# Performance work log

Hardware: AMD Instinct MI355X
Metric: run time of the kernel (lower is better)

The kernel has to match this reference:

```python
import jax, jax.numpy as jnp
import numpy as np

DIM = 128
HEADS = 4
DIM_HEAD = 32
HIDDEN = HEADS * DIM_HEAD  # 128
EPS = 1e-5


def setup_inputs() -> dict:
    key = jax.random.key(0)
    k0, k1, k2, k3 = jax.random.split(key, 4)
    b, h, w = 8, 128, 128
    x = jax.random.normal(k0, (b, DIM, h, w), dtype=jnp.float32)
    # 1x1 conv weights stored as [out_ch, in_ch]
    w_qkv = jax.random.normal(k1, (HIDDEN * 3, DIM), dtype=jnp.float32) * (1.0 / np.sqrt(DIM))
    w_out = jax.random.normal(k2, (DIM, HIDDEN), dtype=jnp.float32) * (1.0 / np.sqrt(HIDDEN))
    b_out = jnp.zeros((DIM,), dtype=jnp.float32)
    alpha = jnp.ones((DIM,), dtype=jnp.float32)
    beta = jnp.zeros((DIM,), dtype=jnp.float32)
    return {"x": x, "w_qkv": w_qkv, "w_out": w_out, "b_out": b_out,
            "alpha": alpha, "beta": beta}


def reference(x, w_qkv, w_out, b_out, alpha, beta):
    b, c, h, w = x.shape
    n = h * w
    scale = DIM_HEAD ** (-0.5)
    # 1x1 conv QKV (bias=False) == channel GEMM
    qkv = jnp.einsum('bchw,oc->bohw', x, w_qkv)  # [b, 3*HIDDEN, h, w]
    q, k, v = jnp.split(qkv, 3, axis=1)
    rs = lambda t: t.reshape(b, HEADS, DIM_HEAD, n)  # [b, heads, d, N]
    q = jax.nn.softmax(rs(q), axis=-2) * scale  # softmax over dim_head axis
    k = jax.nn.softmax(rs(k), axis=-1)          # softmax over spatial axis
    v = rs(v) / n
    # context[dk, dv] = sum_n k[dk, n] * v[dv, n]   (tiny d x d matrix)
    context = jnp.einsum('bhkn,bhvn->bhkv', k, v)
    # out[dv, n] = sum_dk context[dk, dv] * q[dk, n]
    out = jnp.einsum('bhkv,bhkn->bhvn', context, q)
    out = out.reshape(b, HIDDEN, h, w)
    # to_out: 1x1 conv with bias, then channel LayerNorm
    out = jnp.einsum('bchw,oc->bohw', out, w_out) + b_out[None, :, None, None]
    mean = jnp.mean(out, axis=1, keepdims=True)
    var = jnp.var(out, axis=1, keepdims=True)  # unbiased=False
    out = (out - mean) / jnp.sqrt(var + EPS)
    return out * alpha[None, :, None, None] + beta[None, :, None, None]
```

## Files before the change

kernel.cpp:

```cpp
#include <hip/hip_runtime.h>
#include <math.h>

#define B_ 8
#define C_ 128
#define N_ 16384
#define SCALE_ 0.17677669529663687f
#define EPS_ 1e-5f

#define KV_STRIDE 36
#define XU_STRIDE 68
#define REC_ 4224

typedef _Float16 half8 __attribute__((ext_vector_type(8)));
typedef float floatx4 __attribute__((ext_vector_type(4)));

static __device__ inline unsigned short f16bits(float v) {
  _Float16 h = (_Float16)v;
  return __builtin_bit_cast(unsigned short, h);
}

static __device__ inline void pack2(float a0, float a1,
                                    unsigned int& hp, unsigned int& lp) {
  _Float16 h0 = (_Float16)a0;
  _Float16 h1 = (_Float16)a1;
  float l0f = (a0 - (float)h0) * 2048.0f;
  float l1f = (a1 - (float)h1) * 2048.0f;
  hp = ((unsigned int)__builtin_bit_cast(unsigned short, h1) << 16) |
       (unsigned int)__builtin_bit_cast(unsigned short, h0);
  lp = ((unsigned int)f16bits(l1f) << 16) | (unsigned int)f16bits(l0f);
}

static __device__ inline void split8(const float* p, half8& hi, half8& lo) {
  float4 f0 = *(const float4*)p;
  float4 f1 = *(const float4*)(p + 4);
  float fv[8] = {f0.x, f0.y, f0.z, f0.w, f1.x, f1.y, f1.z, f1.w};
#pragma unroll
  for (int j = 0; j < 8; ++j) {
    _Float16 hj = (_Float16)fv[j];
    hi[j] = hj;
    lo[j] = (_Float16)((fv[j] - (float)hj) * 2048.0f);
  }
}

__global__ __launch_bounds__(1024, 4) void lin_attn_ctx(
    const float* __restrict__ x, const float* __restrict__ wqkv,
    float* __restrict__ Ws)
{
  __shared__ __align__(16) unsigned int xhiu[32 * XU_STRIDE];
  __shared__ __align__(16) unsigned int xlou[32 * XU_STRIDE];
  __shared__ __align__(16) float ks[128 * KV_STRIDE];
  __shared__ __align__(16) float vs[128 * KV_STRIDE];

  const int t = threadIdx.x;
  const int bpb = gridDim.x / B_;
  const int b = blockIdx.x / bpb;
  const int blk = blockIdx.x - b * bpb;
  const int nchunks = 512 / bpb;
  const int pbase = blk * (nchunks << 5);

  const int lane = t & 63;
  const int wave = t >> 6;
  const int l15 = lane & 15;
  const int quad = lane >> 4;

  half8 ahi[4], alo[4];
#pragma unroll
  for (int s = 0; s < 4; ++s)
    split8(wqkv + (size_t)(128 + (wave << 4) + l15) * C_ + (s << 5) + (quad << 3),
           ahi[s], alo[s]);

  const int hj = wave >> 2;
  const int at = (wave >> 1) & 1;
  const int bt = wave & 1;
  floatx4 pacc1 = (floatx4){0.f, 0.f, 0.f, 0.f};
  floatx4 pacc2 = (floatx4){0.f, 0.f, 0.f, 0.f};
  float sacc[4] = {0.f, 0.f, 0.f, 0.f};

  const float* xb = x + ((size_t)b * C_) * N_;
  const int kp0 = t >> 4;
  const int pq0 = (t & 15) << 1;

  float2 fa0, fa1;
  {
    const float* p = xb + pbase + pq0;
    fa0 = *(const float2*)(p + (size_t)(2 * kp0) * N_);
    fa1 = *(const float2*)(p + (size_t)(2 * kp0 + 1) * N_);
  }

  for (int c4 = 0; c4 < nchunks; ++c4) {
    __syncthreads();

    half8 eh, el, vh, vl;
    if (c4 > 0) {
      split8(&ks[((hj << 5) + (at << 4) + l15) * KV_STRIDE + (quad << 3)], eh, el);
      split8(&vs[((hj << 5) + (bt << 4) + l15) * KV_STRIDE + (quad << 3)], vh, vl);
    }

    {
      float a0[2] = {fa0.x, fa0.y};
      float a1[2] = {fa1.x, fa1.y};
#pragma unroll
      for (int j = 0; j < 2; ++j) {
        unsigned int hp, lp;
        pack2(a0[j], a1[j], hp, lp);
        xhiu[(pq0 + j) * XU_STRIDE + kp0] = hp;
        xlou[(pq0 + j) * XU_STRIDE + kp0] = lp;
      }
    }

    if (c4 > 0) {
      pacc1 = __builtin_amdgcn_mfma_f32_16x16x32_f16(eh, vh, pacc1, 0, 0, 0);
      pacc2 = __builtin_amdgcn_mfma_f32_16x16x32_f16(eh, vl, pacc2, 0, 0, 0);
      pacc2 = __builtin_amdgcn_mfma_f32_16x16x32_f16(el, vh, pacc2, 0, 0, 0);
    }

    __syncthreads();

    if (c4 + 1 < nchunks) {
      const float* p = xb + pbase + ((c4 + 1) << 5) + pq0;
      fa0 = *(const float2*)(p + (size_t)(2 * kp0) * N_);
      fa1 = *(const float2*)(p + (size_t)(2 * kp0 + 1) * N_);
    }

    floatx4 acc1[2], acc2[2];
#pragma unroll
    for (int c = 0; c < 2; ++c) {
      acc1[c] = (floatx4){0.f, 0.f, 0.f, 0.f};
      acc2[c] = (floatx4){0.f, 0.f, 0.f, 0.f};
    }
    __builtin_amdgcn_s_setprio(1);
#pragma unroll
    for (int s = 0; s < 4; ++s) {
#pragma unroll
      for (int c = 0; c < 2; ++c) {
        int off = ((c << 4) + l15) * XU_STRIDE + (s << 4) + (quad << 2);
        half8 bh = __builtin_bit_cast(half8, *(const uint4*)&xhiu[off]);
        half8 bl = __builtin_bit_cast(half8, *(const uint4*)&xlou[off]);
        acc1[c] = __builtin_amdgcn_mfma_f32_16x16x32_f16(ahi[s], bh, acc1[c], 0, 0, 0);
        acc2[c] = __builtin_amdgcn_mfma_f32_16x16x32_f16(ahi[s], bl, acc2[c], 0, 0, 0);
        acc2[c] = __builtin_amdgcn_mfma_f32_16x16x32_f16(alo[s], bh, acc2[c], 0, 0, 0);
      }
    }
    __builtin_amdgcn_s_setprio(0);

    if (wave < 8) {
#pragma unroll
      for (int c = 0; c < 2; ++c) {
        int px = (c << 4) + l15;
#pragma unroll
        for (int reg = 0; reg < 4; ++reg) {
          float val = acc1[c][reg] + acc2[c][reg] * (1.0f / 2048.0f);
          int row = (wave << 4) + (quad << 2) + reg;
          float e = __expf(val);
          ks[row * KV_STRIDE + px] = e;
          sacc[reg] += e;
        }
      }
    } else {
#pragma unroll
      for (int c = 0; c < 2; ++c) {
        int px = (c << 4) + l15;
#pragma unroll
        for (int reg = 0; reg < 4; ++reg) {
          float val = acc1[c][reg] + acc2[c][reg] * (1.0f / 2048.0f);
          int row = ((wave - 8) << 4) + (quad << 2) + reg;
          vs[row * KV_STRIDE + px] = val;
        }
      }
    }
  }

  __syncthreads();
  {
    half8 eh, el, vh, vl;
    split8(&ks[((hj << 5) + (at << 4) + l15) * KV_STRIDE + (quad << 3)], eh, el);
    split8(&vs[((hj << 5) + (bt << 4) + l15) * KV_STRIDE + (quad << 3)], vh, vl);
    pacc1 = __builtin_amdgcn_mfma_f32_16x16x32_f16(eh, vh, pacc1, 0, 0, 0);
    pacc2 = __builtin_amdgcn_mfma_f32_16x16x32_f16(eh, vl, pacc2, 0, 0, 0);
    pacc2 = __builtin_amdgcn_mfma_f32_16x16x32_f16(el, vh, pacc2, 0, 0, 0);
  }

  {
    float* rec = Ws + (size_t)blockIdx.x * REC_;
#pragma unroll
    for (int reg = 0; reg < 4; ++reg) {
      int dk = (at << 4) + (quad << 2) + reg;
      int dv = (bt << 4) + l15;
      rec[(((hj << 5) + dk) << 5) + dv] =
          pacc1[reg] + pacc2[reg] * (1.0f / 2048.0f);
    }
    if (wave < 8) {
#pragma unroll
      for (int reg = 0; reg < 4; ++reg) {
        float s = sacc[reg];
        s += __shfl_xor(s, 1);
        s += __shfl_xor(s, 2);
        s += __shfl_xor(s, 4);
        s += __shfl_xor(s, 8);
        sacc[reg] = s;
      }
      if (l15 == 0) {
#pragma unroll
        for (int reg = 0; reg < 4; ++reg)
          rec[4096 + (wave << 4) + (quad << 2) + reg] = sacc[reg];
      }
    }
  }
}

__global__ void lin_attn_redg(const float* __restrict__ Ws, int slots,
                              const float* __restrict__ wout,
                              float* __restrict__ G)
{
  __shared__ float p2[256];
  __shared__ float cx[128];
  __shared__ float ss[4];

  const int t = threadIdx.x;
  const int b = blockIdx.x >> 5;
  const int seg = blockIdx.x & 31;
  const int R0 = seg << 2;
  const int hs = slots >> 1;

  {
    const int e = t & 127;
    const int half = t >> 7;
    const float* src = Ws + ((size_t)b * slots + (size_t)half * hs) * REC_ +
                       R0 * 32 + e;
    float s = 0.f;
    for (int k = 0; k < hs; ++k) s += src[(size_t)k * REC_];
    p2[half * 128 + e] = s;
  }
  {
    const int row4 = t >> 6;
    const int lane = t & 63;
    float sv = (lane < slots)
             ? Ws[((size_t)b * slots + lane) * REC_ + 4096 + R0 + row4] : 0.f;
    sv += __shfl_xor(sv, 1);
    sv += __shfl_xor(sv, 2);
    sv += __shfl_xor(sv, 4);
    sv += __shfl_xor(sv, 8);
    sv += __shfl_xor(sv, 16);
    sv += __shfl_xor(sv, 32);
    if (lane == 0) ss[row4] = sv;
  }
  __syncthreads();
  if (t < 128) {
    cx[t] = (p2[t] + p2[128 + t]) / (ss[t >> 5] * 16384.f);
  }
  __syncthreads();
  {
    const int o = t >> 1;
    const int pr = t & 1;
#pragma unroll
    for (int p = 0; p < 2; ++p) {
      const int row4 = pr * 2 + p;
      const int grow = R0 + row4;
      const int h = grow >> 5;
      const float* wrow = wout + (size_t)o * 128 + h * 32;
      const float* crow = &cx[row4 * 32];
      float s = 0.f;
#pragma unroll
      for (int q = 0; q < 8; ++q) {
        float4 w4 = *(const float4*)&wrow[q * 4];
        float4 c4 = *(const float4*)&crow[q * 4];
        s += w4.x * c4.x + w4.y * c4.y + w4.z * c4.z + w4.w * c4.w;
      }
      G[(size_t)b * 16384 + (size_t)o * 128 + grow] = s * SCALE_;
    }
  }
}

__global__ __launch_bounds__(1024, 4) void lin_attn_out(
    const float* __restrict__ x, const float* __restrict__ wqkv,
    const float* __restrict__ G, const float* __restrict__ bout,
    const float* __restrict__ alpha, const float* __restrict__ beta,
    float* __restrict__ out)
{
  __shared__ __align__(16) unsigned int xh[2][32 * XU_STRIDE];
  __shared__ __align__(16) unsigned int xl[2][32 * XU_STRIDE];
  __shared__ __align__(16) unsigned int qhiu[32 * XU_STRIDE];
  __shared__ __align__(16) unsigned int qlou[32 * XU_STRIDE];
  __shared__ float ssum[256];
  __shared__ float red_s[2][256];
  __shared__ float red_q[2][256];

  const int t = threadIdx.x;
  const int bpb = gridDim.x / B_;
  const int b = blockIdx.x / bpb;
  const int blk = blockIdx.x - b * bpb;
  const int nchunks = 512 / bpb;
  const int pbase = blk * (nchunks << 5);

  const int lane = t & 63;
  const int wave = t >> 6;
  const int l15 = lane & 15;
  const int quad = lane >> 4;
  const bool qw = (wave < 8);
  const int yw = wave - 8;

  half8 ahi[4], alo[4];
  {
    const float* base = qw
        ? (wqkv + (size_t)((wave << 4) + l15) * C_)
        : (G + (size_t)b * 16384 + (size_t)((yw << 4) + l15) * 128);
#pragma unroll
    for (int s = 0; s < 4; ++s)
      split8(base + (s << 5) + (quad << 3), ahi[s], alo[s]);
  }

  float bch[4], ach[4], bech[4];
  if (!qw) {
#pragma unroll
    for (int reg = 0; reg < 4; ++reg) {
      int ch = (yw << 4) + (quad << 2) + reg;
      bch[reg] = bout[ch];
      ach[reg] = alpha[ch];
      bech[reg] = beta[ch];
    }
  }

  const float* xb = x + ((size_t)b * C_) * N_;
  float* ob0 = out + ((size_t)b * C_) * N_ + pbase;
  const int kp0 = t >> 4;
  const int pq0 = (t & 15) << 1;

  float2 fa0, fa1;
  {
    const float* p = xb + pbase + pq0;
    fa0 = *(const float2*)(p + (size_t)(2 * kp0) * N_);
    fa1 = *(const float2*)(p + (size_t)(2 * kp0 + 1) * N_);
    float a0[2] = {fa0.x, fa0.y};
    float a1[2] = {fa1.x, fa1.y};
#pragma unroll
    for (int j = 0; j < 2; ++j) {
      unsigned int hp, lp;
      pack2(a0[j], a1[j], hp, lp);
      xh[0][(pq0 + j) * XU_STRIDE + kp0] = hp;
      xl[0][(pq0 + j) * XU_STRIDE + kp0] = lp;
    }
  }

  float eq[2][4];
  float sown[2];
  float yv[2][4];

  for (int i = 0; i <= nchunks; ++i) {
    __syncthreads();

    if (i + 1 < nchunks) {
      const float* p = xb + pbase + ((i + 1) << 5) + pq0;
      fa0 = *(const float2*)(p + (size_t)(2 * kp0) * N_);
      fa1 = *(const float2*)(p + (size_t)(2 * kp0 + 1) * N_);
    }

    if (qw) {
      if (i < nchunks) {
        const int cur = i & 1;
        floatx4 a1c[2], a2c[2];
#pragma unroll
        for (int c = 0; c < 2; ++c) {
          a1c[c] = (floatx4){0.f, 0.f, 0.f, 0.f};
          a2c[c] = (floatx4){0.f, 0.f, 0.f, 0.f};
        }
        __builtin_amdgcn_s_setprio(1);
#pragma unroll
        for (int s = 0; s < 4; ++s) {
#pragma unroll
          for (int c = 0; c < 2; ++c) {
            int off = ((c << 4) + l15) * XU_STRIDE + (s << 4) + (quad << 2);
            half8 bh = __builtin_bit_cast(half8, *(const uint4*)&xh[cur][off]);
            half8 bl = __builtin_bit_cast(half8, *(const uint4*)&xl[cur][off]);
            a1c[c] = __builtin_amdgcn_mfma_f32_16x16x32_f16(ahi[s], bh, a1c[c], 0, 0, 0);
            a2c[c] = __builtin_amdgcn_mfma_f32_16x16x32_f16(ahi[s], bl, a2c[c], 0, 0, 0);
            a2c[c] = __builtin_amdgcn_mfma_f32_16x16x32_f16(alo[s], bh, a2c[c], 0, 0, 0);
          }
        }
        __builtin_amdgcn_s_setprio(0);
#pragma unroll
        for (int c = 0; c < 2; ++c) {
          float s4 = 0.f;
#pragma unroll
          for (int reg = 0; reg < 4; ++reg) {
            float v = a1c[c][reg] + a2c[c][reg] * (1.0f / 2048.0f);
            float e = __expf(v);
            eq[c][reg] = e;
            s4 += e;
          }
          s4 += __shfl_xor(s4, 16);
          s4 += __shfl_xor(s4, 32);
          sown[c] = s4;
          if (quad == 0) ssum[(wave << 5) + (c << 4) + l15] = s4;
        }
      }
    } else {
      if (i >= 2) {
        const float* rs = red_s[i & 1];
        const float* rq = red_q[i & 1];
        float* ob = ob0 + ((i - 2) << 5);
#pragma unroll
        for (int c = 0; c < 2; ++c) {
          int px = (c << 4) + l15;
          float ts = ((rs[px] + rs[32 + px]) + (rs[64 + px] + rs[96 + px])) +
                     ((rs[128 + px] + rs[160 + px]) + (rs[192 + px] + rs[224 + px]));
          float tq = ((rq[px] + rq[32 + px]) + (rq[64 + px] + rq[96 + px])) +
                     ((rq[128 + px] + rq[160 + px]) + (rq[192 + px] + rq[224 + px]));
          float mean = ts * (1.f / 128.f);
          float var = tq * (1.f / 128.f) - mean * mean;
          float rstd = 1.f / sqrtf(var + EPS_);
#pragma unroll
          for (int reg = 0; reg < 4; ++reg) {
            int ch = (yw << 4) + (quad << 2) + reg;
            ob[(size_t)ch * N_ + px] =
                (yv[c][reg] - mean) * rstd * ach[reg] + bech[reg];
          }
        }
      }
      if (i >= 1) {
        floatx4 a1c[2], a2c[2];
#pragma unroll
        for (int c = 0; c < 2; ++c) {
          a1c[c] = (floatx4){0.f, 0.f, 0.f, 0.f};
          a2c[c] = (floatx4){0.f, 0.f, 0.f, 0.f};
        }
        __builtin_amdgcn_s_setprio(1);
#pragma unroll
        for (int s = 0; s < 4; ++s) {
#pragma unroll
          for (int c = 0; c < 2; ++c) {
            int off = ((c << 4) + l15) * XU_STRIDE + (s << 4) + (quad << 2);
            half8 bh = __builtin_bit_cast(half8, *(const uint4*)&qhiu[off]);
            half8 bl = __builtin_bit_cast(half8, *(const uint4*)&qlou[off]);
            a1c[c] = __builtin_amdgcn_mfma_f32_16x16x32_f16(ahi[s], bh, a1c[c], 0, 0, 0);
            a2c[c] = __builtin_amdgcn_mfma_f32_16x16x32_f16(ahi[s], bl, a2c[c], 0, 0, 0);
            a2c[c] = __builtin_amdgcn_mfma_f32_16x16x32_f16(alo[s], bh, a2c[c], 0, 0, 0);
          }
        }
        __builtin_amdgcn_s_setprio(0);
        const int cb = (i - 1) & 1;
#pragma unroll
        for (int c = 0; c < 2; ++c) {
          float sm = 0.f, sq = 0.f;
#pragma unroll
          for (int reg = 0; reg < 4; ++reg) {
            float v = a1c[c][reg] + a2c[c][reg] * (1.0f / 2048.0f) + bch[reg];
            yv[c][reg] = v;
            sm += v;
            sq += v * v;
          }
          sm += __shfl_xor(sm, 16);  sq += __shfl_xor(sq, 16);
          sm += __shfl_xor(sm, 32);  sq += __shfl_xor(sq, 32);
          if (quad == 0) {
            red_s[cb][(yw << 5) + (c << 4) + l15] = sm;
            red_q[cb][(yw << 5) + (c << 4) + l15] = sq;
          }
        }
      }
    }

    if (i + 1 < nchunks) {
      const int nx = (i + 1) & 1;
      float a0[2] = {fa0.x, fa0.y};
      float a1[2] = {fa1.x, fa1.y};
#pragma unroll
      for (int j = 0; j < 2; ++j) {
        unsigned int hp, lp;
        pack2(a0[j], a1[j], hp, lp);
        xh[nx][(pq0 + j) * XU_STRIDE + kp0] = hp;
        xl[nx][(pq0 + j) * XU_STRIDE + kp0] = lp;
      }
    }

    __syncthreads();

    if (qw && i < nchunks) {
#pragma unroll
      for (int c = 0; c < 2; ++c) {
        int px = (c << 4) + l15;
        float pairs = ssum[((wave ^ 1) << 5) + (c << 4) + l15];
        float inv = 1.0f / (sown[c] + pairs);
        unsigned int h0, l0, h1, l1;
        pack2(eq[c][0] * inv, eq[c][1] * inv, h0, l0);
        pack2(eq[c][2] * inv, eq[c][3] * inv, h1, l1);
        int kp = (wave << 3) + (quad << 1);
        uint2 hu; hu.x = h0; hu.y = h1;
        uint2 lu; lu.x = l0; lu.y = l1;
        *(uint2*)&qhiu[px * XU_STRIDE + kp] = hu;
        *(uint2*)&qlou[px * XU_STRIDE + kp] = lu;
      }
    }
  }

  __syncthreads();
  if (!qw) {
    const float* rs = red_s[(nchunks - 1) & 1];
    const float* rq = red_q[(nchunks - 1) & 1];
    float* ob = ob0 + ((nchunks - 1) << 5);
#pragma unroll
    for (int c = 0; c < 2; ++c) {
      int px = (c << 4) + l15;
      float ts = ((rs[px] + rs[32 + px]) + (rs[64 + px] + rs[96 + px])) +
                 ((rs[128 + px] + rs[160 + px]) + (rs[192 + px] + rs[224 + px]));
      float tq = ((rq[px] + rq[32 + px]) + (rq[64 + px] + rq[96 + px])) +
                 ((rq[128 + px] + rq[160 + px]) + (rq[192 + px] + rq[224 + px]));
      float mean = ts * (1.f / 128.f);
      float var = tq * (1.f / 128.f) - mean * mean;
      float rstd = 1.f / sqrtf(var + EPS_);
#pragma unroll
      for (int reg = 0; reg < 4; ++reg) {
        int ch = (yw << 4) + (quad << 2) + reg;
        ob[(size_t)ch * N_ + px] =
            (yv[c][reg] - mean) * rstd * ach[reg] + bech[reg];
      }
    }
  }
}

extern "C" void kernel_launch(void* const* d_in, const int* in_sizes, int n_in,
                              void* d_out, int out_size, void* d_ws, size_t ws_size,
                              hipStream_t stream) {
  const float* x     = (const float*)d_in[0];
  const float* wqkv  = (const float*)d_in[1];
  const float* wout  = (const float*)d_in[2];
  const float* bout  = (const float*)d_in[3];
  const float* alpha = (const float*)d_in[4];
  const float* beta  = (const float*)d_in[5];
  float* outp = (float*)d_out;

  float* G  = (float*)d_ws;
  float* Ws = G + (size_t)B_ * 16384 + B_ * 4096 + B_ * 128;

  const int bpb_ctx = 32;

  lin_attn_ctx<<<dim3(B_ * bpb_ctx), dim3(1024), 0, stream>>>(x, wqkv, Ws);
  lin_attn_redg<<<dim3(B_ * 32), dim3(256), 0, stream>>>(Ws, bpb_ctx, wout, G);
  lin_attn_out<<<dim3(B_ * 32), dim3(1024), 0, stream>>>(x, wqkv, G, bout,
                                                         alpha, beta, outp);
}
```

Baseline: 212.2 us.

## Deepen chunk pipeline to one barrier per iteration with double-buffered q tiles

Restructures the main loop of the output kernel so each chunk iteration needs only one __syncthreads instead of two. The q-normalisation store moves to the start of the next iteration, and the q tiles and softmax partial sums become double-buffered. The pipeline grows by one stage, so the output-GEMM and LayerNorm waves lag two chunks behind. The x staging loads are also narrowed to the upper 512 threads, each doing float4 loads, which frees the q-softmax waves from global load work. In exchange the kernel uses more LDS and runs extra drain iterations, which may reduce occupancy.

```diff
diff --git a/kernel.cpp b/kernel.cpp
--- a/kernel.cpp
+++ b/kernel.cpp
@@ -279,9 +279,9 @@
 {
   __shared__ __align__(16) unsigned int xh[2][32 * XU_STRIDE];
   __shared__ __align__(16) unsigned int xl[2][32 * XU_STRIDE];
-  __shared__ __align__(16) unsigned int qhiu[32 * XU_STRIDE];
-  __shared__ __align__(16) unsigned int qlou[32 * XU_STRIDE];
-  __shared__ float ssum[256];
+  __shared__ __align__(16) unsigned int qh[2][32 * XU_STRIDE];
+  __shared__ __align__(16) unsigned int ql[2][32 * XU_STRIDE];
+  __shared__ float ssum[2][256];
   __shared__ float red_s[2][256];
   __shared__ float red_q[2][256];
 
@@ -322,18 +322,20 @@
 
   const float* xb = x + ((size_t)b * C_) * N_;
   float* ob0 = out + ((size_t)b * C_) * N_ + pbase;
-  const int kp0 = t >> 4;
-  const int pq0 = (t & 15) << 1;
-
-  float2 fa0, fa1;
-  {
+
+  const int st = t - 512;
+  const int kp0 = st >> 3;
+  const int pq0 = (st & 7) << 2;
+
+  float4 fa0, fa1;
+  if (t >= 512) {
     const float* p = xb + pbase + pq0;
-    fa0 = *(const float2*)(p + (size_t)(2 * kp0) * N_);
-    fa1 = *(const float2*)(p + (size_t)(2 * kp0 + 1) * N_);
-    float a0[2] = {fa0.x, fa0.y};
-    float a1[2] = {fa1.x, fa1.y};
-#pragma unroll
-    for (int j = 0; j < 2; ++j) {
+    fa0 = *(const float4*)(p + (size_t)(2 * kp0) * N_);
+    fa1 = *(const float4*)(p + (size_t)(2 * kp0 + 1) * N_);
+    float a0[4] = {fa0.x, fa0.y, fa0.z, fa0.w};
+    float a1[4] = {fa1.x, fa1.y, fa1.z, fa1.w};
+#pragma unroll
+    for (int j = 0; j < 4; ++j) {
       unsigned int hp, lp;
       pack2(a0[j], a1[j], hp, lp);
       xh[0][(pq0 + j) * XU_STRIDE + kp0] = hp;
@@ -345,16 +347,33 @@
   float sown[2];
   float yv[2][4];
 
-  for (int i = 0; i <= nchunks; ++i) {
+  for (int i = 0; i <= nchunks + 2; ++i) {
     __syncthreads();
 
-    if (i + 1 < nchunks) {
+    if (t >= 512 && i + 1 < nchunks) {
       const float* p = xb + pbase + ((i + 1) << 5) + pq0;
-      fa0 = *(const float2*)(p + (size_t)(2 * kp0) * N_);
-      fa1 = *(const float2*)(p + (size_t)(2 * kp0 + 1) * N_);
+      fa0 = *(const float4*)(p + (size_t)(2 * kp0) * N_);
+      fa1 = *(const float4*)(p + (size_t)(2 * kp0 + 1) * N_);
     }
 
     if (qw) {
+      if (i >= 1 && i - 1 < nchunks) {
+        const int pe = (i - 1) & 1;
+#pragma unroll
+        for (int c = 0; c < 2; ++c) {
+          int px = (c << 4) + l15;
+          float pairs = ssum[pe][((wave ^ 1) << 5) + (c << 4) + l15];
+          float inv = 1.0f / (sown[c] + pairs);
+          unsigned int h0, l0, h1, l1;
+          pack2(eq[c][0] * inv, eq[c][1] * inv, h0, l0);
+          pack2(eq[c][2] * inv, eq[c][3] * inv, h1, l1);
+          int kp = (wave << 3) + (quad << 1);
+          uint2 hu; hu.x = h0; hu.y = h1;
+          uint2 lu; lu.x = l0; lu.y = l1;
+          *(uint2*)&qh[pe][px * XU_STRIDE + kp] = hu;
+          *(uint2*)&ql[pe][px * XU_STRIDE + kp] = lu;
+        }
+      }
       if (i < nchunks) {
         const int cur = i & 1;
         floatx4 a1c[2], a2c[2];
@@ -390,14 +409,15 @@
           s4 += __shfl_xor(s4, 16);
           s4 += __shfl_xor(s4, 32);
           sown[c] = s4;
-          if (quad == 0) ssum[(wave << 5) + (c << 4) + l15] = s4;
+          if (quad == 0) ssum[i & 1][(wave << 5) + (c << 4) + l15] = s4;
         }
       }
     } else {
-      if (i >= 2) {
-        const float* rs = red_s[i & 1];
-        const float* rq = red_q[i & 1];
-        float* ob = ob0 + ((i - 2) << 5);
+      if (i >= 3) {
+        const int pf = (i - 3) & 1;
+        const float* rs = red_s[pf];
+        const float* rq = red_q[pf];
+        float* ob = ob0 + ((i - 3) << 5);
 #pragma unroll
         for (int c = 0; c < 2; ++c) {
           int px = (c << 4) + l15;
@@ -416,7 +436,8 @@
           }
         }
       }
-      if (i >= 1) {
+      if (i >= 2 && i - 2 < nchunks) {
+        const int pe = i & 1;
         floatx4 a1c[2], a2c[2];
 #pragma unroll
         for (int c = 0; c < 2; ++c) {
@@ -429,15 +450,14 @@
 #pragma unroll
           for (int c = 0; c < 2; ++c) {
             int off = ((c << 4) + l15) * XU_STRIDE + (s << 4) + (quad << 2);
-            half8 bh = __builtin_bit_cast(half8, *(const uint4*)&qhiu[off]);
-            half8 bl = __builtin_bit_cast(half8, *(const uint4*)&qlou[off]);
+            half8 bh = __builtin_bit_cast(half8, *(const uint4*)&qh[pe][off]);
+            half8 bl = __builtin_bit_cast(half8, *(const uint4*)&ql[pe][off]);
             a1c[c] = __builtin_amdgcn_mfma_f32_16x16x32_f16(ahi[s], bh, a1c[c], 0, 0, 0);
             a2c[c] = __builtin_amdgcn_mfma_f32_16x16x32_f16(ahi[s], bl, a2c[c], 0, 0, 0);
             a2c[c] = __builtin_amdgcn_mfma_f32_16x16x32_f16(alo[s], bh, a2c[c], 0, 0, 0);
           }
         }
         __builtin_amdgcn_s_setprio(0);
-        const int cb = (i - 1) & 1;
 #pragma unroll
         for (int c = 0; c < 2; ++c) {
           float sm = 0.f, sq = 0.f;
@@ -451,66 +471,23 @@
           sm += __shfl_xor(sm, 16);  sq += __shfl_xor(sq, 16);
           sm += __shfl_xor(sm, 32);  sq += __shfl_xor(sq, 32);
           if (quad == 0) {
-            red_s[cb][(yw << 5) + (c << 4) + l15] = sm;
-            red_q[cb][(yw << 5) + (c << 4) + l15] = sq;
+            red_s[pe][(yw << 5) + (c << 4) + l15] = sm;
+            red_q[pe][(yw << 5) + (c << 4) + l15] = sq;
           }
         }
       }
     }
 
-    if (i + 1 < nchunks) {
+    if (t >= 512 && i + 1 < nchunks) {
       const int nx = (i + 1) & 1;
-      float a0[2] = {fa0.x, fa0.y};
-      float a1[2] = {fa1.x, fa1.y};
-#pragma unroll
-      for (int j = 0; j < 2; ++j) {
+      float a0[4] = {fa0.x, fa0.y, fa0.z, fa0.w};
+      float a1[4] = {fa1.x, fa1.y, fa1.z, fa1.w};
+#pragma unroll
+      for (int j = 0; j < 4; ++j) {
         unsigned int hp, lp;
         pack2(a0[j], a1[j], hp, lp);
         xh[nx][(pq0 + j) * XU_STRIDE + kp0] = hp;
         xl[nx][(pq0 + j) * XU_STRIDE + kp0] = lp;
-      }
-    }
-
-    __syncthreads();
-
-    if (qw && i < nchunks) {
-#pragma unroll
-      for (int c = 0; c < 2; ++c) {
-        int px = (c << 4) + l15;
-        float pairs = ssum[((wave ^ 1) << 5) + (c << 4) + l15];
-        float inv = 1.0f / (sown[c] + pairs);
-        unsigned int h0, l0, h1, l1;
-        pack2(eq[c][0] * inv, eq[c][1] * inv, h0, l0);
-        pack2(eq[c][2] * inv, eq[c][3] * inv, h1, l1);
-        int kp = (wave << 3) + (quad << 1);
-        uint2 hu; hu.x = h0; hu.y = h1;
-        uint2 lu; lu.x = l0; lu.y = l1;
-        *(uint2*)&qhiu[px * XU_STRIDE + kp] = hu;
-        *(uint2*)&qlou[px * XU_STRIDE + kp] = lu;
-      }
-    }
-  }
-
-  __syncthreads();
-  if (!qw) {
-    const float* rs = red_s[(nchunks - 1) & 1];
-    const float* rq = red_q[(nchunks - 1) & 1];
-    float* ob = ob0 + ((nchunks - 1) << 5);
-#pragma unroll
-    for (int c = 0; c < 2; ++c) {
-      int px = (c << 4) + l15;
-      float ts = ((rs[px] + rs[32 + px]) + (rs[64 + px] + rs[96 + px])) +
-                 ((rs[128 + px] + rs[160 + px]) + (rs[192 + px] + rs[224 + px]));
-      float tq = ((rq[px] + rq[32 + px]) + (rq[64 + px] + rq[96 + px])) +
-                 ((rq[128 + px] + rq[160 + px]) + (rq[192 + px] + rq[224 + px]));
-      float mean = ts * (1.f / 128.f);
-      float var = tq * (1.f / 128.f) - mean * mean;
-      float rstd = 1.f / sqrtf(var + EPS_);
-#pragma unroll
-      for (int reg = 0; reg < 4; ++reg) {
-        int ch = (yw << 4) + (quad << 2) + reg;
-        ob[(size_t)ch * N_ + px] =
-            (yv[c][reg] - mean) * rstd * ach[reg] + bech[reg];
       }
     }
   }
```

Result: faster. 199.9 us (-5.8%).
